# Kernel tuning notes

Hardware: AMD Instinct MI355X
Metric: run time of the kernel (lower is better)

The kernel has to match this reference:

```python
import jax, jax.numpy as jnp
import numpy as np

N = 262144   # batch of states
D = 32       # in_dim

def setup_inputs() -> dict:
    key = jax.random.key(0)
    k1, k2 = jax.random.split(key)
    x = jax.random.normal(k1, (N, D), dtype=jnp.float32)
    # learned bilinear tensor W[k, i, j], as in nn.Parameter(Tensor(D, D, D))
    weight = jax.random.normal(k2, (D, D, D), dtype=jnp.float32) * (1.0 / np.sqrt(D))
    return {"x": x, "weight": weight}

def reference(x, weight):
    # torch: xBx = x @ W @ x.T -> (D, N, N); out = diagonal(xBx.permute(2,1,0)).t()
    # i.e. out[n, k] = sum_{i,j} x[n,i] * W[k,i,j] * x[n,j]
    # Compute the batched quadratic form directly, skipping the (D, N, N) tensor.
    xW = jnp.einsum('ni,kij->nkj', x, weight)   # (N, D, D) intermediate
    out = jnp.einsum('nkj,nj->nk', xW, x)       # (N, D)
    return out
```

## Files before the change

### kernel.cpp

```cpp
#include <hip/hip_runtime.h>


typedef _Float16 f16x2 __attribute__((ext_vector_type(2)));
typedef _Float16 f16x4 __attribute__((ext_vector_type(4)));
typedef _Float16 f16x8 __attribute__((ext_vector_type(8)));
typedef float    f32x16 __attribute__((ext_vector_type(16)));

static __device__ __forceinline__ unsigned int pk2_f16(float lo, float hi) {
    return __builtin_bit_cast(unsigned int, __builtin_amdgcn_cvt_pkrtz(lo, hi));
}
static __device__ __forceinline__ f16x2 u2h(unsigned int u) {
    return __builtin_bit_cast(f16x2, u);
}
static __device__ __forceinline__ unsigned short f16b(float f) {
    _Float16 h = (_Float16)f;
    return __builtin_bit_cast(unsigned short, h);
}

__global__ __launch_bounds__(256)
void prep_btab_sym(const float* __restrict__ W, unsigned short* __restrict__ bt) {
    __shared__ float Wlds[1024];
    const int k = blockIdx.x;
    const int t = threadIdx.x;
    {
        const float4* src = (const float4*)(W + k * 1024);
        ((float4*)Wlds)[t] = src[t];
    }
    __syncthreads();
    if (t < 66) {
        int n  = t >> 1;
        int lh = t & 1;
        int d  = (n == 32) ? 16 : (n >> 1);
        int q  = (n == 32) ? 0  : (n & 1);
        unsigned short v[8];
        #pragma unroll
        for (int b = 0; b < 8; ++b) {
            int i = q * 16 + lh * 8 + b;
            int j = (i + d) & 31;
            float s = (d == 0) ? Wlds[i * 32 + i]
                               : Wlds[i * 32 + j] + Wlds[j * 32 + i];
            v[b] = f16b(s);
        }
        uint4 pk;
        pk.x = (unsigned int)v[0] | ((unsigned int)v[1] << 16);
        pk.y = (unsigned int)v[2] | ((unsigned int)v[3] << 16);
        pk.z = (unsigned int)v[4] | ((unsigned int)v[5] << 16);
        pk.w = (unsigned int)v[6] | ((unsigned int)v[7] << 16);
        ((uint4*)bt)[n * 64 + k + lh * 32] = pk;
    }
}

#define XS 18

__global__ __launch_bounds__(512, 8)
void quadform_kernel(const float* __restrict__ x,
                     const unsigned short* __restrict__ bt_ws,
                     float* __restrict__ out) {
    __shared__ __align__(16) unsigned short btab[33 * 64 * 8];
    __shared__ __align__(16) unsigned int   xstage[256 * XS];

    const int tid  = threadIdx.x;
    const int lane = tid & 63;
    const int wave = tid >> 6;
    const int hi   = lane >> 5;
    const int rl   = lane & 31;
    const long blockrow = (long)blockIdx.x * 256;
    const long wrow = blockrow + wave * 32;

    const float4* xsrc = (const float4*)(x + blockrow * 32);
    float4 xg0 = xsrc[tid];
    float4 xg1 = xsrc[512 + tid];
    float4 xg2 = xsrc[1024 + tid];
    float4 xg3 = xsrc[1536 + tid];

    const uint4* bsrc = (const uint4*)bt_ws;
    uint4* bdst = (uint4*)btab;
    {
        uint4 b0 = bsrc[tid];
        uint4 b1 = bsrc[512 + tid];
        bdst[tid]       = b0;
        bdst[512 + tid] = b1;
    }

    #pragma unroll
    for (int c = 0; c < 4; ++c) {
        float4 v = (c == 0) ? xg0 : (c == 1) ? xg1 : (c == 2) ? xg2 : xg3;
        int idx = c * 512 + tid;
        int row = idx >> 3;
        int sub = idx & 7;
        uint2 w2;
        w2.x = pk2_f16(v.x, v.y);
        w2.y = pk2_f16(v.z, v.w);
        *(uint2*)&xstage[row * XS + sub * 2] = w2;
    }

    {
        uint4 b2 = bsrc[1024 + tid];
        uint4 b3 = bsrc[1536 + tid];
        bdst[1024 + tid] = b2;
        bdst[1536 + tid] = b3;
        if (tid < 64) bdst[2048 + tid] = bsrc[2048 + tid];
    }
    __syncthreads();

    unsigned int ypk[16];
    {
        unsigned int xpk[16];
        const unsigned int* xr = &xstage[(wave * 32 + rl) * XS];
        #pragma unroll
        for (int c = 0; c < 4; ++c) {
            uint4 v = *(const uint4*)(xr + c * 4);
            xpk[c * 4 + 0] = v.x;
            xpk[c * 4 + 1] = v.y;
            xpk[c * 4 + 2] = v.z;
            xpk[c * 4 + 3] = v.w;
        }
        #pragma unroll
        for (int c = 0; c < 16; ++c)
            ypk[c] = hi ? xpk[(c + 4) & 15] : xpk[c];
    }

    f32x16 acc;
    #pragma unroll
    for (int e = 0; e < 16; ++e) acc[e] = 0.0f;

    #pragma unroll
    for (int s = 0; s < 33; ++s) {
        const int d   = (s == 32) ? 16 : (s >> 1);
        const int q8  = ((s == 32) ? 0 : (s & 1)) * 8;
        const int dh  = d >> 1;
        const bool od = (d & 1) != 0;
        f16x8 bfrag = *(const f16x8*)(&btab[(s * 64 + lane) * 8]);

        f16x2 b0 = od ? u2h(__builtin_amdgcn_perm(ypk[(q8 + 0 + dh + 1) & 15], ypk[(q8 + 0 + dh) & 15], 0x05040302u)) : u2h(ypk[(q8 + 0 + dh) & 15]);
        f16x2 b1 = od ? u2h(__builtin_amdgcn_perm(ypk[(q8 + 1 + dh + 1) & 15], ypk[(q8 + 1 + dh) & 15], 0x05040302u)) : u2h(ypk[(q8 + 1 + dh) & 15]);
        f16x2 b2 = od ? u2h(__builtin_amdgcn_perm(ypk[(q8 + 2 + dh + 1) & 15], ypk[(q8 + 2 + dh) & 15], 0x05040302u)) : u2h(ypk[(q8 + 2 + dh) & 15]);
        f16x2 b3 = od ? u2h(__builtin_amdgcn_perm(ypk[(q8 + 3 + dh + 1) & 15], ypk[(q8 + 3 + dh) & 15], 0x05040302u)) : u2h(ypk[(q8 + 3 + dh) & 15]);
        f16x2 a0 = u2h(ypk[q8 + 0]) * b0;
        f16x2 a1 = u2h(ypk[q8 + 1]) * b1;
        f16x2 a2 = u2h(ypk[q8 + 2]) * b2;
        f16x2 a3 = u2h(ypk[q8 + 3]) * b3;
        f16x4 lo = __builtin_shufflevector(a0, a1, 0, 1, 2, 3);
        f16x4 hf = __builtin_shufflevector(a2, a3, 0, 1, 2, 3);
        f16x8 a  = __builtin_shufflevector(lo, hf, 0, 1, 2, 3, 4, 5, 6, 7);
        acc = __builtin_amdgcn_mfma_f32_32x32x16_f16(a, bfrag, acc, 0, 0, 0);
    }

    float* ob = out + (wrow + 4 * hi) * 32 + rl;
    #pragma unroll
    for (int e = 0; e < 16; ++e)
        __builtin_nontemporal_store(acc[e], ob + (e & 3) * 32 + (e >> 2) * 256);
}

extern "C" void kernel_launch(void* const* d_in, const int* in_sizes, int n_in,
                              void* d_out, int out_size, void* d_ws, size_t ws_size,
                              hipStream_t stream) {
    const float* x = (const float*)d_in[0];
    const float* W = (const float*)d_in[1];
    float* out = (float*)d_out;
    unsigned short* bt = (unsigned short*)d_ws;

    prep_btab_sym<<<32, 256, 0, stream>>>(W, bt);
    int nrows = in_sizes[0] / 32;
    int grid  = nrows / 256;
    quadform_kernel<<<grid, 512, 0, stream>>>(x, bt, out);
}
```

Before: 23.76 us.

## Process two 256-row chunks per block to amortize B-table staging

Each block now handles 512 rows instead of 256. It loads all x for both chunks up front into two shared-memory staging buffers, then runs the MFMA quadratic-form loop twice while reusing the shared B table. This halves the number of times the 33 KB coefficient table is copied from global memory into LDS across the grid. In exchange, register and LDS use per block rise, occupancy drops (launch bounds go from 8 to 4), the grid is halved, and more loads are in flight per thread.

```diff
diff --git a/kernel.cpp b/kernel.cpp
--- a/kernel.cpp
+++ b/kernel.cpp
@@ -52,34 +52,88 @@
 
 #define XS 18
 
-__global__ __launch_bounds__(512, 8)
+#define CHUNK_COMPUTE(YSTAGE, WROW)                                              \
+    {                                                                            \
+        unsigned int ypk[16];                                                    \
+        {                                                                        \
+            unsigned int xpk[16];                                                \
+            const unsigned int* xr = &(YSTAGE)[(wave * 32 + rl) * XS];           \
+            _Pragma("unroll")                                                    \
+            for (int c = 0; c < 4; ++c) {                                        \
+                uint4 v = *(const uint4*)(xr + c * 4);                           \
+                xpk[c * 4 + 0] = v.x; xpk[c * 4 + 1] = v.y;                      \
+                xpk[c * 4 + 2] = v.z; xpk[c * 4 + 3] = v.w;                      \
+            }                                                                    \
+            _Pragma("unroll")                                                    \
+            for (int c = 0; c < 16; ++c)                                         \
+                ypk[c] = hi ? xpk[(c + 4) & 15] : xpk[c];                        \
+        }                                                                        \
+        f32x16 acc;                                                              \
+        _Pragma("unroll")                                                        \
+        for (int e = 0; e < 16; ++e) acc[e] = 0.0f;                              \
+        _Pragma("unroll")                                                        \
+        for (int s = 0; s < 33; ++s) {                                           \
+            const int d   = (s == 32) ? 16 : (s >> 1);                           \
+            const int q8  = ((s == 32) ? 0 : (s & 1)) * 8;                       \
+            const int dh  = d >> 1;                                              \
+            const bool od = (d & 1) != 0;                                        \
+            f16x8 bfrag = *(const f16x8*)(&btab[(s * 64 + lane) * 8]);           \
+            f16x2 b0 = od ? u2h(__builtin_amdgcn_perm(ypk[(q8 + 0 + dh + 1) & 15], ypk[(q8 + 0 + dh) & 15], 0x05040302u)) : u2h(ypk[(q8 + 0 + dh) & 15]); \
+            f16x2 b1 = od ? u2h(__builtin_amdgcn_perm(ypk[(q8 + 1 + dh + 1) & 15], ypk[(q8 + 1 + dh) & 15], 0x05040302u)) : u2h(ypk[(q8 + 1 + dh) & 15]); \
+            f16x2 b2 = od ? u2h(__builtin_amdgcn_perm(ypk[(q8 + 2 + dh + 1) & 15], ypk[(q8 + 2 + dh) & 15], 0x05040302u)) : u2h(ypk[(q8 + 2 + dh) & 15]); \
+            f16x2 b3 = od ? u2h(__builtin_amdgcn_perm(ypk[(q8 + 3 + dh + 1) & 15], ypk[(q8 + 3 + dh) & 15], 0x05040302u)) : u2h(ypk[(q8 + 3 + dh) & 15]); \
+            f16x2 a0 = u2h(ypk[q8 + 0]) * b0;                                    \
+            f16x2 a1 = u2h(ypk[q8 + 1]) * b1;                                    \
+            f16x2 a2 = u2h(ypk[q8 + 2]) * b2;                                    \
+            f16x2 a3 = u2h(ypk[q8 + 3]) * b3;                                    \
+            f16x4 lo = __builtin_shufflevector(a0, a1, 0, 1, 2, 3);              \
+            f16x4 hf = __builtin_shufflevector(a2, a3, 0, 1, 2, 3);              \
+            f16x8 a  = __builtin_shufflevector(lo, hf, 0, 1, 2, 3, 4, 5, 6, 7);  \
+            acc = __builtin_amdgcn_mfma_f32_32x32x16_f16(a, bfrag, acc, 0, 0, 0);\
+        }                                                                        \
+        float* ob = out + ((WROW) + 4 * hi) * 32 + rl;                           \
+        _Pragma("unroll")                                                        \
+        for (int e = 0; e < 16; ++e)                                             \
+            __builtin_nontemporal_store(acc[e], ob + (e & 3) * 32 + (e >> 2) * 256); \
+    }
+
+__global__ __launch_bounds__(512, 4)
 void quadform_kernel(const float* __restrict__ x,
                      const unsigned short* __restrict__ bt_ws,
                      float* __restrict__ out) {
     __shared__ __align__(16) unsigned short btab[33 * 64 * 8];
-    __shared__ __align__(16) unsigned int   xstage[256 * XS];
+    __shared__ __align__(16) unsigned int   xstage0[256 * XS];
+    __shared__ __align__(16) unsigned int   xstage1[256 * XS];
 
     const int tid  = threadIdx.x;
     const int lane = tid & 63;
     const int wave = tid >> 6;
     const int hi   = lane >> 5;
     const int rl   = lane & 31;
-    const long blockrow = (long)blockIdx.x * 256;
-    const long wrow = blockrow + wave * 32;
+    const long blockrow = (long)blockIdx.x * 512;
 
     const float4* xsrc = (const float4*)(x + blockrow * 32);
     float4 xg0 = xsrc[tid];
     float4 xg1 = xsrc[512 + tid];
     float4 xg2 = xsrc[1024 + tid];
     float4 xg3 = xsrc[1536 + tid];
+    float4 xg4 = xsrc[2048 + tid];
+    float4 xg5 = xsrc[2560 + tid];
+    float4 xg6 = xsrc[3072 + tid];
+    float4 xg7 = xsrc[3584 + tid];
 
     const uint4* bsrc = (const uint4*)bt_ws;
     uint4* bdst = (uint4*)btab;
     {
         uint4 b0 = bsrc[tid];
         uint4 b1 = bsrc[512 + tid];
-        bdst[tid]       = b0;
-        bdst[512 + tid] = b1;
+        uint4 b2 = bsrc[1024 + tid];
+        uint4 b3 = bsrc[1536 + tid];
+        bdst[tid]        = b0;
+        bdst[512 + tid]  = b1;
+        bdst[1024 + tid] = b2;
+        bdst[1536 + tid] = b3;
+        if (tid < 64) bdst[2048 + tid] = bsrc[2048 + tid];
     }
 
     #pragma unroll
@@ -91,65 +145,23 @@
         uint2 w2;
         w2.x = pk2_f16(v.x, v.y);
         w2.y = pk2_f16(v.z, v.w);
-        *(uint2*)&xstage[row * XS + sub * 2] = w2;
+        *(uint2*)&xstage0[row * XS + sub * 2] = w2;
     }
-
-    {
-        uint4 b2 = bsrc[1024 + tid];
-        uint4 b3 = bsrc[1536 + tid];
-        bdst[1024 + tid] = b2;
-        bdst[1536 + tid] = b3;
-        if (tid < 64) bdst[2048 + tid] = bsrc[2048 + tid];
+    #pragma unroll
+    for (int c = 0; c < 4; ++c) {
+        float4 v = (c == 0) ? xg4 : (c == 1) ? xg5 : (c == 2) ? xg6 : xg7;
+        int idx = c * 512 + tid;
+        int row = idx >> 3;
+        int sub = idx & 7;
+        uint2 w2;
+        w2.x = pk2_f16(v.x, v.y);
+        w2.y = pk2_f16(v.z, v.w);
+        *(uint2*)&xstage1[row * XS + sub * 2] = w2;
     }
     __syncthreads();
 
-    unsigned int ypk[16];
-    {
-        unsigned int xpk[16];
-        const unsigned int* xr = &xstage[(wave * 32 + rl) * XS];
-        #pragma unroll
-        for (int c = 0; c < 4; ++c) {
-            uint4 v = *(const uint4*)(xr + c * 4);
-            xpk[c * 4 + 0] = v.x;
-            xpk[c * 4 + 1] = v.y;
-            xpk[c * 4 + 2] = v.z;
-            xpk[c * 4 + 3] = v.w;
-        }
-        #pragma unroll
-        for (int c = 0; c < 16; ++c)
-            ypk[c] = hi ? xpk[(c + 4) & 15] : xpk[c];
-    }
-
-    f32x16 acc;
-    #pragma unroll
-    for (int e = 0; e < 16; ++e) acc[e] = 0.0f;
-
-    #pragma unroll
-    for (int s = 0; s < 33; ++s) {
-        const int d   = (s == 32) ? 16 : (s >> 1);
-        const int q8  = ((s == 32) ? 0 : (s & 1)) * 8;
-        const int dh  = d >> 1;
-        const bool od = (d & 1) != 0;
-        f16x8 bfrag = *(const f16x8*)(&btab[(s * 64 + lane) * 8]);
-
-        f16x2 b0 = od ? u2h(__builtin_amdgcn_perm(ypk[(q8 + 0 + dh + 1) & 15], ypk[(q8 + 0 + dh) & 15], 0x05040302u)) : u2h(ypk[(q8 + 0 + dh) & 15]);
-        f16x2 b1 = od ? u2h(__builtin_amdgcn_perm(ypk[(q8 + 1 + dh + 1) & 15], ypk[(q8 + 1 + dh) & 15], 0x05040302u)) : u2h(ypk[(q8 + 1 + dh) & 15]);
-        f16x2 b2 = od ? u2h(__builtin_amdgcn_perm(ypk[(q8 + 2 + dh + 1) & 15], ypk[(q8 + 2 + dh) & 15], 0x05040302u)) : u2h(ypk[(q8 + 2 + dh) & 15]);
-        f16x2 b3 = od ? u2h(__builtin_amdgcn_perm(ypk[(q8 + 3 + dh + 1) & 15], ypk[(q8 + 3 + dh) & 15], 0x05040302u)) : u2h(ypk[(q8 + 3 + dh) & 15]);
-        f16x2 a0 = u2h(ypk[q8 + 0]) * b0;
-        f16x2 a1 = u2h(ypk[q8 + 1]) * b1;
-        f16x2 a2 = u2h(ypk[q8 + 2]) * b2;
-        f16x2 a3 = u2h(ypk[q8 + 3]) * b3;
-        f16x4 lo = __builtin_shufflevector(a0, a1, 0, 1, 2, 3);
-        f16x4 hf = __builtin_shufflevector(a2, a3, 0, 1, 2, 3);
-        f16x8 a  = __builtin_shufflevector(lo, hf, 0, 1, 2, 3, 4, 5, 6, 7);
-        acc = __builtin_amdgcn_mfma_f32_32x32x16_f16(a, bfrag, acc, 0, 0, 0);
-    }
-
-    float* ob = out + (wrow + 4 * hi) * 32 + rl;
-    #pragma unroll
-    for (int e = 0; e < 16; ++e)
-        __builtin_nontemporal_store(acc[e], ob + (e & 3) * 32 + (e >> 2) * 256);
+    CHUNK_COMPUTE(xstage0, blockrow + wave * 32)
+    CHUNK_COMPUTE(xstage1, blockrow + 256 + wave * 32)
 }
 
 extern "C" void kernel_launch(void* const* d_in, const int* in_sizes, int n_in,
@@ -162,6 +174,6 @@
 
     prep_btab_sym<<<32, 256, 0, stream>>>(W, bt);
     int nrows = in_sizes[0] / 32;
-    int grid  = nrows / 256;
+    int grid  = nrows / 512;
     quadform_kernel<<<grid, 512, 0, stream>>>(x, bt, out);
 }
```

After: 23.84 us. About the same (+0.4%).
